# Optimization experiments

Measured on AMD Instinct MI355X. Metric: run time of the kernel, lower is better.

Reference implementation:

```python
import jax, jax.numpy as jnp
import numpy as np

B = 512        # batch
P = 32 * 6 * 6 # 1152 primary capsules
C = 10         # digit capsules (n_caps)
D = 16         # output capsule dim (n_dims)
IN = 8         # primary capsule dim
ITERS = 3      # routing iterations


def setup_inputs() -> dict:
    key = jax.random.key(0)
    k1, k2 = jax.random.split(key)
    x = jax.random.normal(k1, (B, P, IN), dtype=jnp.float32)
    # routing_weights param (leading batch-1 dim squeezed; broadcast replaces repeat)
    W = jax.random.normal(k2, (P, C, D, IN), dtype=jnp.float32)
    return {"x": x, "W": W}


def squash(t, axis=-1, eps=1e-7):
    sq = jnp.sum(t * t, axis=axis, keepdims=True)
    return (sq / (1.0 + sq)) * t / jnp.sqrt(sq + eps)


def reference(x, W):
    # prediction vectors u_hat: [B, P, C, D]  (equiv to W@x with repeats replaced by einsum)
    u_hat = jnp.einsum('pcdi,bpi->bpcd', W, x)
    logits = jnp.zeros((B, P, C), dtype=x.dtype)
    v = None
    for i in range(ITERS):
        coup = jax.nn.softmax(logits, axis=2)                  # over n_caps, matches dim=2
        s = jnp.einsum('bpc,bpcd->bcd', coup, u_hat)           # sum over primary caps (dim=1)
        v = squash(s, axis=-1)                                 # squash over capsule dim (torch dim=-2)
        if i != ITERS - 1:
            agreement = jnp.einsum('bpcd,bcd->bpc', u_hat, v)  # u_hat^T @ v
            logits = logits + agreement
    # match torch output shape [B, 1, C, D, 1]
    return v[:, None, :, :, None]
```

## Files before the change

kernel.cpp:

```cpp
#include <hip/hip_runtime.h>
#include <hip/hip_bf16.h>

#define NB 512
#define NP 1152
#define NC 10
#define ND 16
#define NI 8

constexpr int K_B    = 2;
constexpr int B_TILE = 4 * 4 * K_B;
constexpr int P_TILE = 8;
constexpr int NBLK_B = NB / B_TILE;
constexpr int NBLK_P = NP / P_TILE;
constexpr int SVD = NB * NC * ND;
constexpr int W_TILE_BYTES = P_TILE * NC * ND * NI * 4;
constexpr int X_TILE_FLOATS = B_TILE * P_TILE * NI;

constexpr float LOG2E = 1.4426950408889634f;

typedef float v2f __attribute__((ext_vector_type(2)));

__device__ __forceinline__ float red16_dpp(float v) {
    int t;
    t = __builtin_amdgcn_update_dpp(0, __float_as_int(v), 0xB1, 0xF, 0xF, true);
    v += __int_as_float(t);
    t = __builtin_amdgcn_update_dpp(0, __float_as_int(v), 0x4E, 0xF, 0xF, true);
    v += __int_as_float(t);
    t = __builtin_amdgcn_update_dpp(0, __float_as_int(v), 0x124, 0xF, 0xF, true);
    v += __int_as_float(t);
    t = __builtin_amdgcn_update_dpp(0, __float_as_int(v), 0x128, 0xF, 0xF, true);
    v += __int_as_float(t);
    return v;
}

template<int PASS, bool TS>
__global__ __launch_bounds__(256, 2)
void caps_pass(const float* __restrict__ x,
               const float* __restrict__ w,
               const float* __restrict__ v0,
               const float* __restrict__ v1,
               float* __restrict__ s_out)
{
    __shared__ __align__(16) float w_lds[W_TILE_BYTES / 4];
    __shared__ __align__(16) float x_lds[X_TILE_FLOATS];

    const int tid  = threadIdx.x;
    const int lane = tid & 63;
    const int wave = tid >> 6;
    const int d    = lane & 15;
    const int bsub = lane >> 4;
    const int bblk = blockIdx.x % NBLK_B;
    const int pblk = blockIdx.x / NBLK_B;
    const int p0   = pblk * P_TILE;

    {
        const uint8_t* wsrc = (const uint8_t*)w + (size_t)pblk * W_TILE_BYTES;
        const int lane_src = (lane << 4) ^ ((lane & 8) << 1) ^ ((lane & 16) << 1);
        #pragma unroll
        for (int j = 0; j < 10; ++j) {
            const int off = wave * 10240 + j * 1024;
            __builtin_amdgcn_global_load_lds(
                (const __attribute__((address_space(1))) void*)(wsrc + off + lane_src),
                (__attribute__((address_space(3))) void*)((uint8_t*)w_lds + off),
                16, 0, 0);
        }
    }

    {
        #pragma unroll
        for (int j = 0; j < 2; ++j) {
            const int u   = wave * 128 + j * 64 + lane;
            const int bl  = u >> 4;
            const int w16 = u & 15;
            const float* bbase = x + ((size_t)(bblk * B_TILE + bl) * NP + p0) * NI;
            const uint8_t* src = (const uint8_t*)bbase + ((w16 ^ (bl & 3)) * 16);
            __builtin_amdgcn_global_load_lds(
                (const __attribute__((address_space(1))) void*)src,
                (__attribute__((address_space(3))) void*)((uint8_t*)x_lds + (size_t)u * 16),
                16, 0, 0);
        }
    }

    int bidx[K_B];
    #pragma unroll
    for (int k = 0; k < K_B; ++k) bidx[k] = bblk * B_TILE + wave * 8 + k * 4 + bsub;

    float vr[K_B][NC];
    if (PASS >= 1) {
        #pragma unroll
        for (int k = 0; k < K_B; ++k)
            #pragma unroll
            for (int c = 0; c < NC; ++c) {
                float vv = v0[(bidx[k] * NC + c) * ND + d];
                if (PASS == 2) vv += v1[(bidx[k] * NC + c) * ND + d];
                vr[k][c] = vv * LOG2E;
            }
    }

    float sacc[K_B][NC];
    #pragma unroll
    for (int k = 0; k < K_B; ++k)
        #pragma unroll
        for (int c = 0; c < NC; ++c) sacc[k][c] = 0.0f;

    const int lane_rd = (d << 5) ^ ((d & 4) << 2) ^ ((d & 8) << 2);
    const int xswz    = bsub << 4;

    asm volatile("s_waitcnt vmcnt(0)" ::: "memory");
    __syncthreads();

    for (int pp = 0; pp < P_TILE; ++pp) {
        v2f xv[K_B][4];
        #pragma unroll
        for (int k = 0; k < K_B; ++k) {
            const int xb = ((wave * 8 + k * 4 + bsub) * 256 + pp * 32) ^ xswz;
            const uint8_t* xp = (const uint8_t*)x_lds;
            const float4 a = *(const float4*)(xp + xb);
            const float4 b = *(const float4*)(xp + (xb ^ 16));
            xv[k][0] = v2f{a.x, a.y};
            xv[k][1] = v2f{a.z, a.w};
            xv[k][2] = v2f{b.x, b.y};
            xv[k][3] = v2f{b.z, b.w};
        }

        float uh[K_B][NC];
        #pragma unroll
        for (int c = 0; c < NC; ++c) {
            const uint8_t* pb = (const uint8_t*)w_lds + pp * 5120 + c * 512;
            const float4 wa = *(const float4*)(pb + lane_rd);
            const float4 wb = *(const float4*)(pb + (lane_rd ^ 16));
            const v2f w01{wa.x, wa.y}, w23{wa.z, wa.w};
            const v2f w45{wb.x, wb.y}, w67{wb.z, wb.w};
            #pragma unroll
            for (int k = 0; k < K_B; ++k) {
                v2f acc = w01 * xv[k][0];
                acc = __builtin_elementwise_fma(w23, xv[k][1], acc);
                acc = __builtin_elementwise_fma(w45, xv[k][2], acc);
                acc = __builtin_elementwise_fma(w67, xv[k][3], acc);
                const float u = acc[0] + acc[1];
                if (PASS == 0) sacc[k][c] = fmaf(0.1f, u, sacc[k][c]);
                else           uh[k][c] = u;
            }
        }

        if (PASS >= 1) {
            #pragma unroll
            for (int k = 0; k < K_B; ++k) {
                float lg[NC];
                #pragma unroll
                for (int c = 0; c < NC; ++c)
                    lg[c] = red16_dpp(uh[k][c] * vr[k][c]);
                float ssum = 0.0f;
                float coup[NC];
                #pragma unroll
                for (int c = 0; c < NC; ++c) {
                    coup[c] = __builtin_amdgcn_exp2f(lg[c]);
                    ssum += coup[c];
                }
                const float inv = __builtin_amdgcn_rcpf(ssum);
                #pragma unroll
                for (int c = 0; c < NC; ++c)
                    sacc[k][c] = fmaf(coup[c] * inv, uh[k][c], sacc[k][c]);
            }
        }
    }

    if (TS) {
        float* pout = s_out + (size_t)pblk * SVD;
        #pragma unroll
        for (int k = 0; k < K_B; ++k)
            #pragma unroll
            for (int c = 0; c < NC; ++c)
                pout[(bidx[k] * NC + c) * ND + d] = sacc[k][c];
    } else {
        #pragma unroll
        for (int k = 0; k < K_B; ++k)
            #pragma unroll
            for (int c = 0; c < NC; ++c)
                atomicAdd(&s_out[(bidx[k] * NC + c) * ND + d], sacc[k][c]);
    }
}

__global__ __launch_bounds__(256)
void caps_reduce_squash(const float* __restrict__ part, float* __restrict__ v)
{
    const int idx = blockIdx.x * 256 + threadIdx.x;
    float a0 = 0, a1 = 0, a2 = 0, a3 = 0, a4 = 0, a5 = 0, a6 = 0, a7 = 0;
    #pragma unroll
    for (int r = 0; r < NBLK_P; r += 8) {
        a0 += part[(size_t)(r + 0) * SVD + idx];
        a1 += part[(size_t)(r + 1) * SVD + idx];
        a2 += part[(size_t)(r + 2) * SVD + idx];
        a3 += part[(size_t)(r + 3) * SVD + idx];
        a4 += part[(size_t)(r + 4) * SVD + idx];
        a5 += part[(size_t)(r + 5) * SVD + idx];
        a6 += part[(size_t)(r + 6) * SVD + idx];
        a7 += part[(size_t)(r + 7) * SVD + idx];
    }
    const float sv = ((a0 + a1) + (a2 + a3)) + ((a4 + a5) + (a6 + a7));
    float sq = red16_dpp(sv * sv);
    const float scale = (sq / (1.0f + sq)) / sqrtf(sq + 1e-7f);
    v[idx] = scale * sv;
}

template<bool ZERO_S>
__global__ __launch_bounds__(256)
void caps_squash(float* __restrict__ s, float* __restrict__ v)
{
    const int idx = blockIdx.x * 256 + threadIdx.x;
    const float sv = s[idx];
    if (ZERO_S) s[idx] = 0.0f;
    float sq = red16_dpp(sv * sv);
    const float scale = (sq / (1.0f + sq)) / sqrtf(sq + 1e-7f);
    v[idx] = scale * sv;
}

extern "C" void kernel_launch(void* const* d_in, const int* in_sizes, int n_in,
                              void* d_out, int out_size, void* d_ws, size_t ws_size,
                              hipStream_t stream)
{
    const float* x = (const float*)d_in[0];
    const float* w = (const float*)d_in[1];
    float* out = (float*)d_out;

    const dim3 pgrid(NBLK_B * NBLK_P);
    const dim3 pblock(256);
    const dim3 qgrid(SVD / 256);
    const dim3 qblock(256);

    const size_t partBytes = (size_t)NBLK_P * SVD * sizeof(float);

    if (ws_size >= partBytes + (size_t)SVD * sizeof(float)) {
        float* part = (float*)d_ws;
        float* v0   = (float*)((uint8_t*)d_ws + partBytes);
        float* v1   = out;

        caps_pass<0, true><<<pgrid, pblock, 0, stream>>>(x, w, nullptr, nullptr, part);
        caps_reduce_squash<<<qgrid, qblock, 0, stream>>>(part, v0);
        caps_pass<1, true><<<pgrid, pblock, 0, stream>>>(x, w, v0, nullptr, part);
        caps_reduce_squash<<<qgrid, qblock, 0, stream>>>(part, v1);
        caps_pass<2, true><<<pgrid, pblock, 0, stream>>>(x, w, v0, v1, part);
        caps_reduce_squash<<<qgrid, qblock, 0, stream>>>(part, out);
    } else {
        float* s  = (float*)d_ws;
        float* v0 = s + SVD;
        float* v1 = out;

        hipMemsetAsync(s, 0, (size_t)SVD * sizeof(float), stream);
        caps_pass<0, false><<<pgrid, pblock, 0, stream>>>(x, w, nullptr, nullptr, s);
        caps_squash<true><<<qgrid, qblock, 0, stream>>>(s, v0);
        caps_pass<1, false><<<pgrid, pblock, 0, stream>>>(x, w, v0, nullptr, s);
        caps_squash<true><<<qgrid, qblock, 0, stream>>>(s, v1);
        caps_pass<2, false><<<pgrid, pblock, 0, stream>>>(x, w, v0, v1, s);
        caps_squash<false><<<qgrid, qblock, 0, stream>>>(s, out);
    }
}
```

Measured before the change: 182.4 us.

## Process three P tiles per block to cut partial sums; vectorize reduce

Each block of the routing pass now loops over three consecutive P tiles, reloading the W and x tiles into LDS for each and keeping its accumulators in registers. This cuts the grid and the partial-sum buffer to a third, which reduces the global writes in the pass and the reads in the reduce-squash kernel. The reduce kernel now reads float4 values and uses a 4-lane DPP reduction for the squash norm. In exchange there is less block parallelism and the per-tile loads are serialized inside each block with no prefetch overlap. The atomic fallback path also uses the smaller grid but still accumulates into one buffer, so it stays correct.

```diff
diff --git a/kernel.cpp b/kernel.cpp
--- a/kernel.cpp
+++ b/kernel.cpp
@@ -10,8 +10,10 @@
 constexpr int K_B    = 2;
 constexpr int B_TILE = 4 * 4 * K_B;
 constexpr int P_TILE = 8;
+constexpr int NPT    = 3;
 constexpr int NBLK_B = NB / B_TILE;
 constexpr int NBLK_P = NP / P_TILE;
+constexpr int NBLK_PO = NBLK_P / NPT;
 constexpr int SVD = NB * NC * ND;
 constexpr int W_TILE_BYTES = P_TILE * NC * ND * NI * 4;
 constexpr int X_TILE_FLOATS = B_TILE * P_TILE * NI;
@@ -29,6 +31,15 @@
     t = __builtin_amdgcn_update_dpp(0, __float_as_int(v), 0x124, 0xF, 0xF, true);
     v += __int_as_float(t);
     t = __builtin_amdgcn_update_dpp(0, __float_as_int(v), 0x128, 0xF, 0xF, true);
+    v += __int_as_float(t);
+    return v;
+}
+
+__device__ __forceinline__ float red4_dpp(float v) {
+    int t;
+    t = __builtin_amdgcn_update_dpp(0, __float_as_int(v), 0xB1, 0xF, 0xF, true);
+    v += __int_as_float(t);
+    t = __builtin_amdgcn_update_dpp(0, __float_as_int(v), 0x4E, 0xF, 0xF, true);
     v += __int_as_float(t);
     return v;
 }
@@ -49,37 +60,10 @@
     const int wave = tid >> 6;
     const int d    = lane & 15;
     const int bsub = lane >> 4;
-    const int bblk = blockIdx.x % NBLK_B;
-    const int pblk = blockIdx.x / NBLK_B;
-    const int p0   = pblk * P_TILE;
-
-    {
-        const uint8_t* wsrc = (const uint8_t*)w + (size_t)pblk * W_TILE_BYTES;
-        const int lane_src = (lane << 4) ^ ((lane & 8) << 1) ^ ((lane & 16) << 1);
-        #pragma unroll
-        for (int j = 0; j < 10; ++j) {
-            const int off = wave * 10240 + j * 1024;
-            __builtin_amdgcn_global_load_lds(
-                (const __attribute__((address_space(1))) void*)(wsrc + off + lane_src),
-                (__attribute__((address_space(3))) void*)((uint8_t*)w_lds + off),
-                16, 0, 0);
-        }
-    }
-
-    {
-        #pragma unroll
-        for (int j = 0; j < 2; ++j) {
-            const int u   = wave * 128 + j * 64 + lane;
-            const int bl  = u >> 4;
-            const int w16 = u & 15;
-            const float* bbase = x + ((size_t)(bblk * B_TILE + bl) * NP + p0) * NI;
-            const uint8_t* src = (const uint8_t*)bbase + ((w16 ^ (bl & 3)) * 16);
-            __builtin_amdgcn_global_load_lds(
-                (const __attribute__((address_space(1))) void*)src,
-                (__attribute__((address_space(3))) void*)((uint8_t*)x_lds + (size_t)u * 16),
-                16, 0, 0);
-        }
-    }
+    const int bblk     = blockIdx.x % NBLK_B;
+    const int pblk_out = blockIdx.x / NBLK_B;
+
+    const int lane_src = (lane << 4) ^ ((lane & 8) << 1) ^ ((lane & 16) << 1);
 
     int bidx[K_B];
     #pragma unroll
@@ -106,67 +90,101 @@
     const int lane_rd = (d << 5) ^ ((d & 4) << 2) ^ ((d & 8) << 2);
     const int xswz    = bsub << 4;
 
-    asm volatile("s_waitcnt vmcnt(0)" ::: "memory");
-    __syncthreads();
-
-    for (int pp = 0; pp < P_TILE; ++pp) {
-        v2f xv[K_B][4];
-        #pragma unroll
-        for (int k = 0; k < K_B; ++k) {
-            const int xb = ((wave * 8 + k * 4 + bsub) * 256 + pp * 32) ^ xswz;
-            const uint8_t* xp = (const uint8_t*)x_lds;
-            const float4 a = *(const float4*)(xp + xb);
-            const float4 b = *(const float4*)(xp + (xb ^ 16));
-            xv[k][0] = v2f{a.x, a.y};
-            xv[k][1] = v2f{a.z, a.w};
-            xv[k][2] = v2f{b.x, b.y};
-            xv[k][3] = v2f{b.z, b.w};
+    for (int tt = 0; tt < NPT; ++tt) {
+        const int pblk = pblk_out * NPT + tt;
+        const int p0   = pblk * P_TILE;
+
+        if (tt > 0) __syncthreads();
+
+        {
+            const uint8_t* wsrc = (const uint8_t*)w + (size_t)pblk * W_TILE_BYTES;
+            #pragma unroll
+            for (int j = 0; j < 10; ++j) {
+                const int off = wave * 10240 + j * 1024;
+                __builtin_amdgcn_global_load_lds(
+                    (const __attribute__((address_space(1))) void*)(wsrc + off + lane_src),
+                    (__attribute__((address_space(3))) void*)((uint8_t*)w_lds + off),
+                    16, 0, 0);
+            }
         }
 
-        float uh[K_B][NC];
-        #pragma unroll
-        for (int c = 0; c < NC; ++c) {
-            const uint8_t* pb = (const uint8_t*)w_lds + pp * 5120 + c * 512;
-            const float4 wa = *(const float4*)(pb + lane_rd);
-            const float4 wb = *(const float4*)(pb + (lane_rd ^ 16));
-            const v2f w01{wa.x, wa.y}, w23{wa.z, wa.w};
-            const v2f w45{wb.x, wb.y}, w67{wb.z, wb.w};
+        {
+            #pragma unroll
+            for (int j = 0; j < 2; ++j) {
+                const int u   = wave * 128 + j * 64 + lane;
+                const int bl  = u >> 4;
+                const int w16 = u & 15;
+                const float* bbase = x + ((size_t)(bblk * B_TILE + bl) * NP + p0) * NI;
+                const uint8_t* src = (const uint8_t*)bbase + ((w16 ^ (bl & 3)) * 16);
+                __builtin_amdgcn_global_load_lds(
+                    (const __attribute__((address_space(1))) void*)src,
+                    (__attribute__((address_space(3))) void*)((uint8_t*)x_lds + (size_t)u * 16),
+                    16, 0, 0);
+            }
+        }
+
+        asm volatile("s_waitcnt vmcnt(0)" ::: "memory");
+        __syncthreads();
+
+        for (int pp = 0; pp < P_TILE; ++pp) {
+            v2f xv[K_B][4];
             #pragma unroll
             for (int k = 0; k < K_B; ++k) {
-                v2f acc = w01 * xv[k][0];
-                acc = __builtin_elementwise_fma(w23, xv[k][1], acc);
-                acc = __builtin_elementwise_fma(w45, xv[k][2], acc);
-                acc = __builtin_elementwise_fma(w67, xv[k][3], acc);
-                const float u = acc[0] + acc[1];
-                if (PASS == 0) sacc[k][c] = fmaf(0.1f, u, sacc[k][c]);
-                else           uh[k][c] = u;
+                const int xb = ((wave * 8 + k * 4 + bsub) * 256 + pp * 32) ^ xswz;
+                const uint8_t* xp = (const uint8_t*)x_lds;
+                const float4 a = *(const float4*)(xp + xb);
+                const float4 b = *(const float4*)(xp + (xb ^ 16));
+                xv[k][0] = v2f{a.x, a.y};
+                xv[k][1] = v2f{a.z, a.w};
+                xv[k][2] = v2f{b.x, b.y};
+                xv[k][3] = v2f{b.z, b.w};
+            }
+
+            float uh[K_B][NC];
+            #pragma unroll
+            for (int c = 0; c < NC; ++c) {
+                const uint8_t* pb = (const uint8_t*)w_lds + pp * 5120 + c * 512;
+                const float4 wa = *(const float4*)(pb + lane_rd);
+                const float4 wb = *(const float4*)(pb + (lane_rd ^ 16));
+                const v2f w01{wa.x, wa.y}, w23{wa.z, wa.w};
+                const v2f w45{wb.x, wb.y}, w67{wb.z, wb.w};
+                #pragma unroll
+                for (int k = 0; k < K_B; ++k) {
+                    v2f acc = w01 * xv[k][0];
+                    acc = __builtin_elementwise_fma(w23, xv[k][1], acc);
+                    acc = __builtin_elementwise_fma(w45, xv[k][2], acc);
+                    acc = __builtin_elementwise_fma(w67, xv[k][3], acc);
+                    const float u = acc[0] + acc[1];
+                    if (PASS == 0) sacc[k][c] = fmaf(0.1f, u, sacc[k][c]);
+                    else           uh[k][c] = u;
+                }
+            }
+
+            if (PASS >= 1) {
+                #pragma unroll
+                for (int k = 0; k < K_B; ++k) {
+                    float lg[NC];
+                    #pragma unroll
+                    for (int c = 0; c < NC; ++c)
+                        lg[c] = red16_dpp(uh[k][c] * vr[k][c]);
+                    float ssum = 0.0f;
+                    float coup[NC];
+                    #pragma unroll
+                    for (int c = 0; c < NC; ++c) {
+                        coup[c] = __builtin_amdgcn_exp2f(lg[c]);
+                        ssum += coup[c];
+                    }
+                    const float inv = __builtin_amdgcn_rcpf(ssum);
+                    #pragma unroll
+                    for (int c = 0; c < NC; ++c)
+                        sacc[k][c] = fmaf(coup[c] * inv, uh[k][c], sacc[k][c]);
+                }
             }
         }
-
-        if (PASS >= 1) {
-            #pragma unroll
-            for (int k = 0; k < K_B; ++k) {
-                float lg[NC];
-                #pragma unroll
-                for (int c = 0; c < NC; ++c)
-                    lg[c] = red16_dpp(uh[k][c] * vr[k][c]);
-                float ssum = 0.0f;
-                float coup[NC];
-                #pragma unroll
-                for (int c = 0; c < NC; ++c) {
-                    coup[c] = __builtin_amdgcn_exp2f(lg[c]);
-                    ssum += coup[c];
-                }
-                const float inv = __builtin_amdgcn_rcpf(ssum);
-                #pragma unroll
-                for (int c = 0; c < NC; ++c)
-                    sacc[k][c] = fmaf(coup[c] * inv, uh[k][c], sacc[k][c]);
-            }
-        }
     }
 
     if (TS) {
-        float* pout = s_out + (size_t)pblk * SVD;
+        float* pout = s_out + (size_t)pblk_out * SVD;
         #pragma unroll
         for (int k = 0; k < K_B; ++k)
             #pragma unroll
@@ -184,23 +202,30 @@
 __global__ __launch_bounds__(256)
 void caps_reduce_squash(const float* __restrict__ part, float* __restrict__ v)
 {
-    const int idx = blockIdx.x * 256 + threadIdx.x;
-    float a0 = 0, a1 = 0, a2 = 0, a3 = 0, a4 = 0, a5 = 0, a6 = 0, a7 = 0;
+    const int g = blockIdx.x * 256 + threadIdx.x;
+    const float4* p4 = (const float4*)part;
+    float4 a0{0,0,0,0}, a1{0,0,0,0}, a2{0,0,0,0}, a3{0,0,0,0};
     #pragma unroll
-    for (int r = 0; r < NBLK_P; r += 8) {
-        a0 += part[(size_t)(r + 0) * SVD + idx];
-        a1 += part[(size_t)(r + 1) * SVD + idx];
-        a2 += part[(size_t)(r + 2) * SVD + idx];
-        a3 += part[(size_t)(r + 3) * SVD + idx];
-        a4 += part[(size_t)(r + 4) * SVD + idx];
-        a5 += part[(size_t)(r + 5) * SVD + idx];
-        a6 += part[(size_t)(r + 6) * SVD + idx];
-        a7 += part[(size_t)(r + 7) * SVD + idx];
-    }
-    const float sv = ((a0 + a1) + (a2 + a3)) + ((a4 + a5) + (a6 + a7));
-    float sq = red16_dpp(sv * sv);
+    for (int r = 0; r < NBLK_PO; r += 4) {
+        const float4 t0 = p4[(size_t)(r + 0) * (SVD / 4) + g];
+        const float4 t1 = p4[(size_t)(r + 1) * (SVD / 4) + g];
+        const float4 t2 = p4[(size_t)(r + 2) * (SVD / 4) + g];
+        const float4 t3 = p4[(size_t)(r + 3) * (SVD / 4) + g];
+        a0.x += t0.x; a0.y += t0.y; a0.z += t0.z; a0.w += t0.w;
+        a1.x += t1.x; a1.y += t1.y; a1.z += t1.z; a1.w += t1.w;
+        a2.x += t2.x; a2.y += t2.y; a2.z += t2.z; a2.w += t2.w;
+        a3.x += t3.x; a3.y += t3.y; a3.z += t3.z; a3.w += t3.w;
+    }
+    float4 sv;
+    sv.x = (a0.x + a1.x) + (a2.x + a3.x);
+    sv.y = (a0.y + a1.y) + (a2.y + a3.y);
+    sv.z = (a0.z + a1.z) + (a2.z + a3.z);
+    sv.w = (a0.w + a1.w) + (a2.w + a3.w);
+    const float sql = ((sv.x * sv.x + sv.y * sv.y) + (sv.z * sv.z + sv.w * sv.w));
+    const float sq  = red4_dpp(sql);
     const float scale = (sq / (1.0f + sq)) / sqrtf(sq + 1e-7f);
-    v[idx] = scale * sv;
+    sv.x *= scale; sv.y *= scale; sv.z *= scale; sv.w *= scale;
+    ((float4*)v)[g] = sv;
 }
 
 template<bool ZERO_S>
@@ -223,12 +248,12 @@
     const float* w = (const float*)d_in[1];
     float* out = (float*)d_out;
 
-    const dim3 pgrid(NBLK_B * NBLK_P);
+    const dim3 pgrid(NBLK_B * NBLK_PO);
     const dim3 pblock(256);
-    const dim3 qgrid(SVD / 256);
-    const dim3 qblock(256);
-
-    const size_t partBytes = (size_t)NBLK_P * SVD * sizeof(float);
+    const dim3 rgrid(SVD / 4 / 256);
+    const dim3 rblock(256);
+
+    const size_t partBytes = (size_t)NBLK_PO * SVD * sizeof(float);
 
     if (ws_size >= partBytes + (size_t)SVD * sizeof(float)) {
         float* part = (float*)d_ws;
@@ -236,15 +261,17 @@
         float* v1   = out;
 
         caps_pass<0, true><<<pgrid, pblock, 0, stream>>>(x, w, nullptr, nullptr, part);
-        caps_reduce_squash<<<qgrid, qblock, 0, stream>>>(part, v0);
+        caps_reduce_squash<<<rgrid, rblock, 0, stream>>>(part, v0);
         caps_pass<1, true><<<pgrid, pblock, 0, stream>>>(x, w, v0, nullptr, part);
-        caps_reduce_squash<<<qgrid, qblock, 0, stream>>>(part, v1);
+        caps_reduce_squash<<<rgrid, rblock, 0, stream>>>(part, v1);
         caps_pass<2, true><<<pgrid, pblock, 0, stream>>>(x, w, v0, v1, part);
-        caps_reduce_squash<<<qgrid, qblock, 0, stream>>>(part, out);
+        caps_reduce_squash<<<rgrid, rblock, 0, stream>>>(part, out);
     } else {
         float* s  = (float*)d_ws;
         float* v0 = s + SVD;
         float* v1 = out;
+        const dim3 qgrid(SVD / 256);
+        const dim3 qblock(256);
 
         hipMemsetAsync(s, 0, (size_t)SVD * sizeof(float), stream);
         caps_pass<0, false><<<pgrid, pblock, 0, stream>>>(x, w, nullptr, nullptr, s);
```

Measured after the change: 244.6 us. 34.1% more time.
